# Kernel optimization log

Hardware: AMD Instinct MI355X
Metric: run time of the kernel (lower is better)

Reference implementation:

```python
import jax, jax.numpy as jnp
import numpy as np

GROUP_SIZE = 32
OUT_FEATURES = 4096
IN_FEATURES = 4096


def _unpack_3bit(p):
    # p: [..., 3] uint8 -> [..., 8] 3-bit values in [0, 7]
    b0, b1, b2 = p[..., 0], p[..., 1], p[..., 2]
    v0 = b0 & 7
    v1 = (b0 >> 3) & 7
    v2 = ((b0 >> 6) & 3) | ((b1 & 1) << 2)
    v3 = (b1 >> 1) & 7
    v4 = (b1 >> 4) & 7
    v5 = ((b1 >> 7) & 1) | ((b2 & 3) << 1)
    v6 = (b2 >> 2) & 7
    v7 = (b2 >> 5) & 7
    return jnp.stack([v0, v1, v2, v3, v4, v5, v6, v7], axis=-1)


def _block_dequantize_3bit(packed, normalization, group_size=GROUP_SIZE):
    # packed: [n_groups, group_size*3//8] int8, normalization: [n_groups, 1]
    p = packed.astype(jnp.uint8).reshape(-1, group_size // 8, 3)
    q = _unpack_3bit(p).reshape(-1, group_size).astype(jnp.float32)
    n = normalization.astype(jnp.float32)  # [n_groups, 1]
    x_norm = q / 7.0
    return (x_norm * (2.0 * n) - n).reshape(-1)


def setup_inputs() -> dict:
    key = jax.random.key(0)
    k1, k2, k3, k4 = jax.random.split(key, 4)
    n_groups = OUT_FEATURES * IN_FEATURES // GROUP_SIZE
    packed_cols = GROUP_SIZE * 3 // 8
    x = jax.random.normal(k1, (2, 2048, IN_FEATURES), dtype=jnp.float32)
    weight_q3 = jax.random.randint(k2, (n_groups, packed_cols), 0, 256, dtype=jnp.int32).astype(jnp.int8)
    weight_norm = jax.random.uniform(k3, (n_groups, 1), dtype=jnp.float32, minval=0.05, maxval=1.0)
    bias = jax.random.normal(k4, (OUT_FEATURES,), dtype=jnp.float32) * 0.02
    return {"x": x, "weight_q3": weight_q3, "weight_norm": weight_norm, "bias": bias}


def reference(x, weight_q3, weight_norm, bias):
    # Dequantize 3-bit packed weights to fp32 [out, in], then F.linear.
    w = _block_dequantize_3bit(weight_q3, weight_norm).reshape(OUT_FEATURES, IN_FEATURES)
    return jnp.einsum('bsi,oi->bso', x, w) + bias
```

## Files before the change

### kernel.cpp

```cpp
#include <hip/hip_runtime.h>
#include <hip/hip_bf16.h>
#include <stdint.h>

#define OUTF 4096
#define INF  4096
#define MROWS 4096
#define GS 32

typedef __attribute__((ext_vector_type(8))) __bf16 bf16x8;
typedef __attribute__((ext_vector_type(4))) float f32x4;

__device__ inline void gload_lds16(const void* g, void* l) {
    __builtin_amdgcn_global_load_lds(
        (const __attribute__((address_space(1))) void*)g,
        (__attribute__((address_space(3))) void*)l, 16, 0, 0);
}

__device__ inline void load_group_bits(const int* __restrict__ wq, int gid,
                                       uint64_t& lo, uint64_t& hi) {
    const int4* p = (const int4*)(wq + (size_t)gid * 12);
    int4 A = p[0], B = p[1], C = p[2];
    uint32_t d0 = (uint32_t)(A.x & 255) | ((uint32_t)(A.y & 255) << 8) |
                  ((uint32_t)(A.z & 255) << 16) | ((uint32_t)(A.w & 255) << 24);
    uint32_t d1 = (uint32_t)(B.x & 255) | ((uint32_t)(B.y & 255) << 8) |
                  ((uint32_t)(B.z & 255) << 16) | ((uint32_t)(B.w & 255) << 24);
    uint32_t d2 = (uint32_t)(C.x & 255) | ((uint32_t)(C.y & 255) << 8) |
                  ((uint32_t)(C.z & 255) << 16) | ((uint32_t)(C.w & 255) << 24);
    lo = (uint64_t)d0 | ((uint64_t)d1 << 32);
    hi = (uint64_t)d1 | ((uint64_t)d2 << 32);
}

__global__ void prep_kernel(const float* __restrict__ x, __bf16* __restrict__ xb,
                            const int* __restrict__ wq, const float* __restrict__ wn,
                            __bf16* __restrict__ wb) {
    const int bid = blockIdx.x;
    if (bid < 8192) {
        int i = bid * 256 + threadIdx.x;
        const f32x4* xp = (const f32x4*)x;
        f32x4 a = xp[2 * i], b = xp[2 * i + 1];
        bf16x8 v = { (__bf16)a[0], (__bf16)a[1], (__bf16)a[2], (__bf16)a[3],
                     (__bf16)b[0], (__bf16)b[1], (__bf16)b[2], (__bf16)b[3] };
        ((bf16x8*)xb)[i] = v;
    } else {
        int gid = (bid - 8192) * 256 + threadIdx.x;
        uint64_t lo, hi;
        load_group_bits(wq, gid, lo, hi);
        float nrm = wn[gid];
        float c2 = nrm * (2.0f / 7.0f), c1 = -nrm;
        bf16x8 o[4];
#pragma unroll
        for (int j = 0; j < 32; ++j) {
            uint32_t q = (j <= 20) ? (uint32_t)((lo >> (3 * j)) & 7)
                                   : (uint32_t)((hi >> (3 * j - 32)) & 7);
            o[j >> 3][j & 7] = (__bf16)((float)q * c2 + c1);
        }
        bf16x8* outp = (bf16x8*)(wb + (size_t)gid * 32);
        outp[0] = o[0]; outp[1] = o[1]; outp[2] = o[2]; outp[3] = o[3];
    }
}


#define RD_A(DST, RB, H) do { \
    _Pragma("unroll") \
    for (int m_ = 0; m_ < 4; ++m_) { \
        const int r_ = wr * 64 + m_ * 16 + row16; \
        _Pragma("unroll") \
        for (int kk_ = 0; kk_ < 2; ++kk_) \
            DST[m_][kk_] = *(const bf16x8*)(lds + (RB) * 65536 + (H) * 16384 + \
                r_ * 128 + (((kk_ * 4 + kq) * 16) ^ ((r_ & 7) << 4))); \
    } \
} while (0)

#define RD_B(DST, RB, H) do { \
    _Pragma("unroll") \
    for (int n_ = 0; n_ < 2; ++n_) { \
        const int r_ = wc * 32 + n_ * 16 + row16; \
        _Pragma("unroll") \
        for (int kk_ = 0; kk_ < 2; ++kk_) \
            DST[n_][kk_] = *(const bf16x8*)(lds + (RB) * 65536 + 32768 + (H) * 16384 + \
                r_ * 128 + (((kk_ * 4 + kq) * 16) ^ ((r_ & 7) << 4))); \
    } \
} while (0)

#define STAGE(SB, AB, H, SKT) do { \
    const __bf16* base_ = (AB) ? wb : xb; \
    const int brc_ = ((AB) ? bn : bm) * 256; \
    _Pragma("unroll") \
    for (int j_ = 0; j_ < 2; ++j_) \
        gload_lds16((const char*)(base_ + (size_t)(brc_ + (H) * 128 + j_ * 64 + srow) * INF + \
                                  (SKT) * 64 + schunk * 8), \
                    lds + (SB) * 65536 + (AB) * 32768 + (H) * 16384 + j_ * 8192 + tid * 16); \
} while (0)

#define MF_Q(A_, B_, MH, NH) do { \
    __builtin_amdgcn_s_setprio(1); \
    _Pragma("unroll") \
    for (int kk_ = 0; kk_ < 2; ++kk_) \
        _Pragma("unroll") \
        for (int m_ = 0; m_ < 4; ++m_) \
            _Pragma("unroll") \
            for (int n_ = 0; n_ < 2; ++n_) \
                acc[MH][NH][m_][n_] = __builtin_amdgcn_mfma_f32_16x16x32_bf16( \
                    A_[m_][kk_], B_[n_][kk_], acc[MH][NH][m_][n_], 0, 0, 0); \
    __builtin_amdgcn_s_setprio(0); \
} while (0)

__global__ __launch_bounds__(512, 2) void gemm8_kernel(
    const __bf16* __restrict__ xb, const __bf16* __restrict__ wb,
    const float* __restrict__ bias, float* __restrict__ out) {
    __shared__ __align__(16) unsigned char lds[131072];

    const int tid = threadIdx.x;
    const int lane = tid & 63, wid = tid >> 6;
    const int wr = wid >> 2, wc = wid & 3;
    const int row16 = lane & 15, kq = lane >> 4;

    const int bid = blockIdx.x;
    const int wg = (bid & 7) * 32 + (bid >> 3);
    const int bn = wg & 15, bm = wg >> 4;

    const int srow = tid >> 3;
    const int schunk = (tid & 7) ^ (srow & 7);

    f32x4 acc[2][2][4][2] = {};
    bf16x8 a[4][2], b0[2][2], b1[2][2];

    STAGE(0, 0, 0, 0); STAGE(0, 1, 0, 0); STAGE(0, 0, 1, 0); STAGE(0, 1, 1, 0);
    __syncthreads();
    RD_A(a, 0, 0); RD_B(b0, 0, 0);

    for (int kt = 0; kt < INF / 64; ++kt) {
        const int rb = kt & 1, sb = rb ^ 1, nt = (kt + 1) & 63;
        STAGE(sb, 0, 0, nt); STAGE(sb, 1, 0, nt);
        STAGE(sb, 0, 1, nt); STAGE(sb, 1, 1, nt);
        RD_B(b1, rb, 1);
        MF_Q(a, b0, 0, 0);
        MF_Q(a, b1, 0, 1);
        RD_A(a, rb, 1);
        MF_Q(a, b1, 1, 1);
        MF_Q(a, b0, 1, 0);
        __syncthreads();
        RD_A(a, sb, 0); RD_B(b0, sb, 0);
    }

#pragma unroll
    for (int nh = 0; nh < 2; ++nh)
#pragma unroll
        for (int n = 0; n < 2; ++n) {
            const int col = bn * 256 + nh * 128 + wc * 32 + n * 16 + row16;
            const float bv = bias[col];
#pragma unroll
            for (int mh = 0; mh < 2; ++mh)
#pragma unroll
                for (int m = 0; m < 4; ++m) {
                    const int rbase = bm * 256 + mh * 128 + wr * 64 + m * 16 + kq * 4;
#pragma unroll
                    for (int j = 0; j < 4; ++j)
                        out[(size_t)(rbase + j) * OUTF + col] = acc[mh][nh][m][n][j] + bv;
                }
        }
}

__global__ __launch_bounds__(256, 2) void gemm_fb_kernel(
    const float* __restrict__ x, const int* __restrict__ wq,
    const float* __restrict__ wn, const float* __restrict__ bias,
    float* __restrict__ out) {
    __shared__ __align__(16) unsigned char lAraw[128 * 128];
    __shared__ __align__(16) unsigned char lBraw[128 * 128];

    const int tid = threadIdx.x;
    const int lane = tid & 63, wid = tid >> 6;
    const int wr = wid >> 1, wc = wid & 1;
    const int bn = blockIdx.x, bm = blockIdx.y;
    const int row16 = lane & 15, kq = lane >> 4;

    f32x4 acc[4][4] = {};

    int aoff[4], boff[4];
#pragma unroll
    for (int m = 0; m < 4; ++m) {
        int r = wr * 64 + m * 16 + row16;
        aoff[m] = r * 128 + ((kq * 16) ^ ((r & 7) << 4));
    }
#pragma unroll
    for (int n = 0; n < 4; ++n) {
        int r = wc * 64 + n * 16 + row16;
        boff[n] = r * 128 + ((kq * 16) ^ ((r & 7) << 4));
    }

    for (int kt = 0; kt < INF / 64; ++kt) {
        __syncthreads();
#pragma unroll
        for (int it = 0; it < 4; ++it) {
            int row = it * 32 + (tid >> 3), c = tid & 7;
            const f32x4* xp = (const f32x4*)(x + (size_t)(bm * 128 + row) * INF + kt * 64 + c * 8);
            f32x4 a0 = xp[0], a1 = xp[1];
            bf16x8 v = { (__bf16)a0[0], (__bf16)a0[1], (__bf16)a0[2], (__bf16)a0[3],
                         (__bf16)a1[0], (__bf16)a1[1], (__bf16)a1[2], (__bf16)a1[3] };
            *(bf16x8*)(lAraw + row * 128 + ((c * 16) ^ ((row & 7) << 4))) = v;
        }
        {
            int row = tid >> 1, gi = tid & 1;
            int gid = (bn * 128 + row) * (INF / GS) + kt * 2 + gi;
            uint64_t lo, hi;
            load_group_bits(wq, gid, lo, hi);
            float nrm = wn[gid];
            float c2 = nrm * (2.0f / 7.0f), c1 = -nrm;
            bf16x8 o[4];
#pragma unroll
            for (int j = 0; j < 32; ++j) {
                uint32_t q = (j <= 20) ? (uint32_t)((lo >> (3 * j)) & 7)
                                       : (uint32_t)((hi >> (3 * j - 32)) & 7);
                o[j >> 3][j & 7] = (__bf16)((float)q * c2 + c1);
            }
            unsigned swz = (row & 7) << 4;
#pragma unroll
            for (int c4 = 0; c4 < 4; ++c4)
                *(bf16x8*)(lBraw + row * 128 + ((gi * 64 + c4 * 16) ^ swz)) = o[c4];
        }
        __syncthreads();

#pragma unroll
        for (int kk = 0; kk < 2; ++kk) {
            bf16x8 afr[4], bfr[4];
#pragma unroll
            for (int m = 0; m < 4; ++m)
                afr[m] = *(const bf16x8*)(lAraw + (aoff[m] ^ (kk * 64)));
#pragma unroll
            for (int n = 0; n < 4; ++n)
                bfr[n] = *(const bf16x8*)(lBraw + (boff[n] ^ (kk * 64)));
#pragma unroll
            for (int m = 0; m < 4; ++m)
#pragma unroll
                for (int n = 0; n < 4; ++n)
                    acc[m][n] = __builtin_amdgcn_mfma_f32_16x16x32_bf16(afr[m], bfr[n], acc[m][n], 0, 0, 0);
        }
    }

#pragma unroll
    for (int n = 0; n < 4; ++n) {
        int col = bn * 128 + wc * 64 + n * 16 + row16;
        float bv = bias[col];
#pragma unroll
        for (int m = 0; m < 4; ++m) {
            int rbase = bm * 128 + wr * 64 + m * 16 + kq * 4;
#pragma unroll
            for (int j = 0; j < 4; ++j)
                out[(size_t)(rbase + j) * OUTF + col] = acc[m][n][j] + bv;
        }
    }
}

extern "C" void kernel_launch(void* const* d_in, const int* in_sizes, int n_in,
                              void* d_out, int out_size, void* d_ws, size_t ws_size,
                              hipStream_t stream) {
    const float* x    = (const float*)d_in[0];
    const int*   wq   = (const int*)d_in[1];
    const float* wn   = (const float*)d_in[2];
    const float* bias = (const float*)d_in[3];
    float* out = (float*)d_out;

    const size_t xb_bytes = (size_t)MROWS * INF * 2;
    const size_t wb_bytes = (size_t)OUTF * INF * 2;
    if (ws_size >= xb_bytes + wb_bytes) {
        __bf16* xb = (__bf16*)d_ws;
        __bf16* wb = (__bf16*)((char*)d_ws + xb_bytes);
        prep_kernel<<<8192 + (OUTF * INF / GS) / 256, 256, 0, stream>>>(x, xb, wq, wn, wb);
        gemm8_kernel<<<(MROWS / 256) * (OUTF / 256), 512, 0, stream>>>(xb, wb, bias, out);
    } else {
        gemm_fb_kernel<<<dim3(OUTF / 128, MROWS / 128), 256, 0, stream>>>(x, wq, wn, bias, out);
    }
}
```

Measured before the change: 145.8 us.

## Interleave staged global loads with MFMA quadrants using fine-grained vmcnt barriers

Restructures the GEMM main loop into four phases. Each phase issues one quarter of the next tile's global-to-LDS loads, reads its LDS fragments, waits on a partial vmcnt, and runs one MFMA quadrant between raw s_barriers. A second A-register set lets both A halves stay live. The goal is to spread memory traffic across compute and replace one heavy __syncthreads with finer waits. The cost is more barriers per iteration, more register pressure, and hand-tuned vmcnt counts that could be wrong for the actual number of outstanding loads.

```diff
diff --git a/kernel.cpp b/kernel.cpp
--- a/kernel.cpp
+++ b/kernel.cpp
@@ -60,6 +60,10 @@
 }
 
 
+#define VMCNT(N) asm volatile("s_waitcnt vmcnt(" #N ")" ::: "memory")
+#define BARR() do { asm volatile("" ::: "memory"); __builtin_amdgcn_s_barrier(); \
+                    asm volatile("" ::: "memory"); } while (0)
+
 #define RD_A(DST, RB, H) do { \
     _Pragma("unroll") \
     for (int m_ = 0; m_ < 4; ++m_) { \
@@ -123,24 +127,36 @@
     const int schunk = (tid & 7) ^ (srow & 7);
 
     f32x4 acc[2][2][4][2] = {};
-    bf16x8 a[4][2], b0[2][2], b1[2][2];
+    bf16x8 a0[4][2], a1[4][2], b0[2][2], b1[2][2];
 
     STAGE(0, 0, 0, 0); STAGE(0, 1, 0, 0); STAGE(0, 0, 1, 0); STAGE(0, 1, 1, 0);
-    __syncthreads();
-    RD_A(a, 0, 0); RD_B(b0, 0, 0);
+    VMCNT(0);
+    BARR();
 
     for (int kt = 0; kt < INF / 64; ++kt) {
         const int rb = kt & 1, sb = rb ^ 1, nt = (kt + 1) & 63;
-        STAGE(sb, 0, 0, nt); STAGE(sb, 1, 0, nt);
-        STAGE(sb, 0, 1, nt); STAGE(sb, 1, 1, nt);
+        STAGE(sb, 0, 0, nt);
+        RD_A(a0, rb, 0); RD_B(b0, rb, 0);
+        VMCNT(4);
+        BARR();
+        MF_Q(a0, b0, 0, 0);
+        BARR();
+        STAGE(sb, 1, 0, nt);
+        RD_A(a1, rb, 1);
+        VMCNT(4);
+        BARR();
+        MF_Q(a1, b0, 1, 0);
+        BARR();
+        STAGE(sb, 0, 1, nt);
         RD_B(b1, rb, 1);
-        MF_Q(a, b0, 0, 0);
-        MF_Q(a, b1, 0, 1);
-        RD_A(a, rb, 1);
-        MF_Q(a, b1, 1, 1);
-        MF_Q(a, b0, 1, 0);
-        __syncthreads();
-        RD_A(a, sb, 0); RD_B(b0, sb, 0);
+        BARR();
+        MF_Q(a1, b1, 1, 1);
+        BARR();
+        STAGE(sb, 1, 1, nt);
+        VMCNT(4);
+        BARR();
+        MF_Q(a0, b1, 0, 1);
+        BARR();
     }
 
 #pragma unroll
```

After: 148.6 us. Within noise of the previous version (+2.0%).

## Replace 256x256 double-buffered GEMM with 256x128 triple-buffered K=32 pipeline

Applied to the files above, without the earlier changes.

The bf16 GEMM moves from 256x256 tiles with K=64 double buffering to 256x128 tiles with K=32 stages in a three-deep LDS ring. Explicit vmcnt waits and raw barriers let two tiles' loads stay in flight, and the smaller LDS footprint allows up to 4 blocks per CU. This trades per-block reuse (more global traffic per FLOP and twice the blocks) for better latency hiding and more occupancy. It also uses a new XOR swizzle for the 64-byte rows.

```diff
diff --git a/kernel.cpp b/kernel.cpp
--- a/kernel.cpp
+++ b/kernel.cpp
@@ -60,105 +60,98 @@
 }
 
 
-#define RD_A(DST, RB, H) do { \
+#define VMCNTQ(N) asm volatile("s_waitcnt vmcnt(" #N ")" ::: "memory")
+#define BARR() do { asm volatile("" ::: "memory"); __builtin_amdgcn_s_barrier(); \
+                    asm volatile("" ::: "memory"); } while (0)
+
+#define STAGE3(SOFF, SKT) do { \
+    gload_lds16(pa0 + (SKT) * 32, lds + (SOFF) + tid * 16); \
+    gload_lds16(pa1 + (SKT) * 32, lds + (SOFF) + 8192 + tid * 16); \
+    gload_lds16(pb0 + (SKT) * 32, lds + (SOFF) + 16384 + tid * 16); \
+} while (0)
+
+#define RD(ROFF) do { \
     _Pragma("unroll") \
-    for (int m_ = 0; m_ < 4; ++m_) { \
-        const int r_ = wr * 64 + m_ * 16 + row16; \
-        _Pragma("unroll") \
-        for (int kk_ = 0; kk_ < 2; ++kk_) \
-            DST[m_][kk_] = *(const bf16x8*)(lds + (RB) * 65536 + (H) * 16384 + \
-                r_ * 128 + (((kk_ * 4 + kq) * 16) ^ ((r_ & 7) << 4))); \
-    } \
+    for (int m_ = 0; m_ < 4; ++m_) \
+        af[m_] = *(const bf16x8*)(lds + (ROFF) + (wr * 64 + m_ * 16 + row16) * 64 + swl); \
+    _Pragma("unroll") \
+    for (int n_ = 0; n_ < 4; ++n_) \
+        bf[n_] = *(const bf16x8*)(lds + (ROFF) + 16384 + (wc * 64 + n_ * 16 + row16) * 64 + swl); \
 } while (0)
 
-#define RD_B(DST, RB, H) do { \
-    _Pragma("unroll") \
-    for (int n_ = 0; n_ < 2; ++n_) { \
-        const int r_ = wc * 32 + n_ * 16 + row16; \
-        _Pragma("unroll") \
-        for (int kk_ = 0; kk_ < 2; ++kk_) \
-            DST[n_][kk_] = *(const bf16x8*)(lds + (RB) * 65536 + 32768 + (H) * 16384 + \
-                r_ * 128 + (((kk_ * 4 + kq) * 16) ^ ((r_ & 7) << 4))); \
-    } \
-} while (0)
-
-#define STAGE(SB, AB, H, SKT) do { \
-    const __bf16* base_ = (AB) ? wb : xb; \
-    const int brc_ = ((AB) ? bn : bm) * 256; \
-    _Pragma("unroll") \
-    for (int j_ = 0; j_ < 2; ++j_) \
-        gload_lds16((const char*)(base_ + (size_t)(brc_ + (H) * 128 + j_ * 64 + srow) * INF + \
-                                  (SKT) * 64 + schunk * 8), \
-                    lds + (SB) * 65536 + (AB) * 32768 + (H) * 16384 + j_ * 8192 + tid * 16); \
-} while (0)
-
-#define MF_Q(A_, B_, MH, NH) do { \
+#define MFMA16() do { \
     __builtin_amdgcn_s_setprio(1); \
     _Pragma("unroll") \
-    for (int kk_ = 0; kk_ < 2; ++kk_) \
+    for (int m_ = 0; m_ < 4; ++m_) \
         _Pragma("unroll") \
-        for (int m_ = 0; m_ < 4; ++m_) \
-            _Pragma("unroll") \
-            for (int n_ = 0; n_ < 2; ++n_) \
-                acc[MH][NH][m_][n_] = __builtin_amdgcn_mfma_f32_16x16x32_bf16( \
-                    A_[m_][kk_], B_[n_][kk_], acc[MH][NH][m_][n_], 0, 0, 0); \
+        for (int n_ = 0; n_ < 4; ++n_) \
+            acc[m_][n_] = __builtin_amdgcn_mfma_f32_16x16x32_bf16( \
+                af[m_], bf[n_], acc[m_][n_], 0, 0, 0); \
     __builtin_amdgcn_s_setprio(0); \
 } while (0)
 
-__global__ __launch_bounds__(512, 2) void gemm8_kernel(
+#define ROT(V) do { (V) += 24576; if ((V) == 3 * 24576) (V) = 0; } while (0)
+
+__global__ __launch_bounds__(512, 4) void gemm3_kernel(
     const __bf16* __restrict__ xb, const __bf16* __restrict__ wb,
     const float* __restrict__ bias, float* __restrict__ out) {
-    __shared__ __align__(16) unsigned char lds[131072];
+    __shared__ __align__(16) unsigned char lds[3 * 24576];
 
     const int tid = threadIdx.x;
     const int lane = tid & 63, wid = tid >> 6;
-    const int wr = wid >> 2, wc = wid & 3;
+    const int wr = wid >> 1, wc = wid & 1;
     const int row16 = lane & 15, kq = lane >> 4;
+    const int swl = (kq ^ ((row16 & 3) ^ ((row16 >> 2) & 3))) * 16;
 
     const int bid = blockIdx.x;
-    const int wg = (bid & 7) * 32 + (bid >> 3);
-    const int bn = wg & 15, bm = wg >> 4;
-
-    const int srow = tid >> 3;
-    const int schunk = (tid & 7) ^ (srow & 7);
-
-    f32x4 acc[2][2][4][2] = {};
-    bf16x8 a[4][2], b0[2][2], b1[2][2];
-
-    STAGE(0, 0, 0, 0); STAGE(0, 1, 0, 0); STAGE(0, 0, 1, 0); STAGE(0, 1, 1, 0);
-    __syncthreads();
-    RD_A(a, 0, 0); RD_B(b0, 0, 0);
-
-    for (int kt = 0; kt < INF / 64; ++kt) {
-        const int rb = kt & 1, sb = rb ^ 1, nt = (kt + 1) & 63;
-        STAGE(sb, 0, 0, nt); STAGE(sb, 1, 0, nt);
-        STAGE(sb, 0, 1, nt); STAGE(sb, 1, 1, nt);
-        RD_B(b1, rb, 1);
-        MF_Q(a, b0, 0, 0);
-        MF_Q(a, b1, 0, 1);
-        RD_A(a, rb, 1);
-        MF_Q(a, b1, 1, 1);
-        MF_Q(a, b0, 1, 0);
-        __syncthreads();
-        RD_A(a, sb, 0); RD_B(b0, sb, 0);
-    }
-
-#pragma unroll
-    for (int nh = 0; nh < 2; ++nh)
-#pragma unroll
-        for (int n = 0; n < 2; ++n) {
-            const int col = bn * 256 + nh * 128 + wc * 32 + n * 16 + row16;
-            const float bv = bias[col];
-#pragma unroll
-            for (int mh = 0; mh < 2; ++mh)
-#pragma unroll
-                for (int m = 0; m < 4; ++m) {
-                    const int rbase = bm * 256 + mh * 128 + wr * 64 + m * 16 + kq * 4;
-#pragma unroll
-                    for (int j = 0; j < 4; ++j)
-                        out[(size_t)(rbase + j) * OUTF + col] = acc[mh][nh][m][n][j] + bv;
-                }
-        }
+    const int wg = (bid & 7) * 64 + (bid >> 3);
+    const int bm = wg >> 5, bn = wg & 31;
+
+    const int ar0 = tid >> 2;
+    const int ac0 = ((tid & 3) ^ ((ar0 & 3) ^ ((ar0 >> 2) & 3))) * 8;
+    const int ar1 = (tid + 512) >> 2;
+    const int ac1 = ((tid & 3) ^ ((ar1 & 3) ^ ((ar1 >> 2) & 3))) * 8;
+    const __bf16* pa0 = xb + (size_t)(bm * 256 + ar0) * INF + ac0;
+    const __bf16* pa1 = xb + (size_t)(bm * 256 + ar1) * INF + ac1;
+    const __bf16* pb0 = wb + (size_t)(bn * 128 + ar0) * INF + ac0;
+
+    f32x4 acc[4][4] = {};
+    bf16x8 af[4], bf[4];
+
+    STAGE3(0, 0);
+    STAGE3(24576, 1);
+
+    int roff = 0, soff = 2 * 24576;
+    for (int kt = 0; kt < 126; ++kt) {
+        VMCNTQ(3);
+        BARR();
+        STAGE3(soff, kt + 2);
+        RD(roff);
+        MFMA16();
+        ROT(roff); ROT(soff);
+    }
+    VMCNTQ(3);
+    BARR();
+    RD(roff);
+    MFMA16();
+    ROT(roff);
+    VMCNTQ(0);
+    BARR();
+    RD(roff);
+    MFMA16();
+
+#pragma unroll
+    for (int n = 0; n < 4; ++n) {
+        const int col = bn * 128 + wc * 64 + n * 16 + row16;
+        const float bv = bias[col];
+#pragma unroll
+        for (int m = 0; m < 4; ++m) {
+            const int rbase = bm * 256 + wr * 64 + m * 16 + kq * 4;
+#pragma unroll
+            for (int j = 0; j < 4; ++j)
+                out[(size_t)(rbase + j) * OUTF + col] = acc[m][n][j] + bv;
+        }
+    }
 }
 
 __global__ __launch_bounds__(256, 2) void gemm_fb_kernel(
@@ -266,7 +259,7 @@
         __bf16* xb = (__bf16*)d_ws;
         __bf16* wb = (__bf16*)((char*)d_ws + xb_bytes);
         prep_kernel<<<8192 + (OUTF * INF / GS) / 256, 256, 0, stream>>>(x, xb, wq, wn, wb);
-        gemm8_kernel<<<(MROWS / 256) * (OUTF / 256), 512, 0, stream>>>(xb, wb, bias, out);
+        gemm3_kernel<<<(MROWS / 256) * (OUTF / 128), 512, 0, stream>>>(xb, wb, bias, out);
     } else {
         gemm_fb_kernel<<<dim3(OUTF / 128, MROWS / 128), 256, 0, stream>>>(x, wq, wn, bias, out);
     }
```

After: 163.6 us. 12.2% more time.

## Split GEMM k-loop barriers with partial vmcnt waits and ping-pong fragments

Applied to the files above, without the earlier changes.

Replaces the single __syncthreads per k-tile with two raw s_barriers, each preceded by a partial s_waitcnt vmcnt. Each barrier waits only for the half of the staged LDS data about to be read. The loop is unrolled by two, with ping-pong A fragment registers and a reordered MFMA/LDS-read schedule. The aim is to overlap global-to-LDS loads with MFMA work instead of draining all loads at every barrier. It relies on hand-counted outstanding load numbers and on the asm barriers for correct ordering, which is fragile if the compiler reorders memory operations.

```diff
diff --git a/kernel.cpp b/kernel.cpp
--- a/kernel.cpp
+++ b/kernel.cpp
@@ -60,6 +60,10 @@
 }
 
 
+#define VMCNT(N) asm volatile("s_waitcnt vmcnt(" #N ")" ::: "memory")
+#define BARR() do { asm volatile("" ::: "memory"); __builtin_amdgcn_s_barrier(); \
+                    asm volatile("" ::: "memory"); } while (0)
+
 #define RD_A(DST, RB, H) do { \
     _Pragma("unroll") \
     for (int m_ = 0; m_ < 4; ++m_) { \
@@ -90,6 +94,11 @@
         gload_lds16((const char*)(base_ + (size_t)(brc_ + (H) * 128 + j_ * 64 + srow) * INF + \
                                   (SKT) * 64 + schunk * 8), \
                     lds + (SB) * 65536 + (AB) * 32768 + (H) * 16384 + j_ * 8192 + tid * 16); \
+} while (0)
+
+#define STAGE_ALL(SB, SKT) do { \
+    STAGE(SB, 0, 0, SKT); STAGE(SB, 1, 0, SKT); \
+    STAGE(SB, 0, 1, SKT); STAGE(SB, 1, 1, SKT); \
 } while (0)
 
 #define MF_Q(A_, B_, MH, NH) do { \
@@ -105,7 +114,20 @@
     __builtin_amdgcn_s_setprio(0); \
 } while (0)
 
-__global__ __launch_bounds__(512, 2) void gemm8_kernel(
+#define TILE(RB, SB, NT, AX, AY) do { \
+    STAGE_ALL(SB, NT); \
+    MF_Q(AX, bP, 0, 0);                \
+    VMCNT(8); BARR(); \
+    RD_A(AY, RB, 1);                   \
+    MF_Q(AY, bP, 1, 0);                \
+    RD_B(bQ, RB, 1);                   \
+    MF_Q(AY, bQ, 1, 1);                \
+    VMCNT(4); BARR(); \
+    RD_A(AY, SB, 0); RD_B(bP, SB, 0);  \
+    MF_Q(AX, bQ, 0, 1);                \
+} while (0)
+
+__global__ __launch_bounds__(512, 2) void gemmP_kernel(
     const __bf16* __restrict__ xb, const __bf16* __restrict__ wb,
     const float* __restrict__ bias, float* __restrict__ out) {
     __shared__ __align__(16) unsigned char lds[131072];
@@ -123,24 +145,16 @@
     const int schunk = (tid & 7) ^ (srow & 7);
 
     f32x4 acc[2][2][4][2] = {};
-    bf16x8 a[4][2], b0[2][2], b1[2][2];
-
-    STAGE(0, 0, 0, 0); STAGE(0, 1, 0, 0); STAGE(0, 0, 1, 0); STAGE(0, 1, 1, 0);
-    __syncthreads();
-    RD_A(a, 0, 0); RD_B(b0, 0, 0);
-
-    for (int kt = 0; kt < INF / 64; ++kt) {
-        const int rb = kt & 1, sb = rb ^ 1, nt = (kt + 1) & 63;
-        STAGE(sb, 0, 0, nt); STAGE(sb, 1, 0, nt);
-        STAGE(sb, 0, 1, nt); STAGE(sb, 1, 1, nt);
-        RD_B(b1, rb, 1);
-        MF_Q(a, b0, 0, 0);
-        MF_Q(a, b1, 0, 1);
-        RD_A(a, rb, 1);
-        MF_Q(a, b1, 1, 1);
-        MF_Q(a, b0, 1, 0);
-        __syncthreads();
-        RD_A(a, sb, 0); RD_B(b0, sb, 0);
+    bf16x8 aP[4][2], aQ[4][2], bP[2][2], bQ[2][2];
+
+    STAGE_ALL(0, 0);
+    VMCNT(4);
+    BARR();
+    RD_A(aP, 0, 0); RD_B(bP, 0, 0);
+
+    for (int kt = 0; kt < INF / 64; kt += 2) {
+        TILE(0, 1, kt + 1, aP, aQ);
+        TILE(1, 0, (kt + 2) & 63, aQ, aP);
     }
 
 #pragma unroll
@@ -266,7 +280,7 @@
         __bf16* xb = (__bf16*)d_ws;
         __bf16* wb = (__bf16*)((char*)d_ws + xb_bytes);
         prep_kernel<<<8192 + (OUTF * INF / GS) / 256, 256, 0, stream>>>(x, xb, wq, wn, wb);
-        gemm8_kernel<<<(MROWS / 256) * (OUTF / 256), 512, 0, stream>>>(xb, wb, bias, out);
+        gemmP_kernel<<<(MROWS / 256) * (OUTF / 256), 512, 0, stream>>>(xb, wb, bias, out);
     } else {
         gemm_fb_kernel<<<dim3(OUTF / 128, MROWS / 128), 256, 0, stream>>>(x, wq, wn, bias, out);
     }
```

New measurement: 284.8 us. 95.3% more time.
